# Optimization experiments

Hardware: AMD Instinct MI355X
Metric: run time of the kernel (lower is better)

## Reference

```python
import jax, jax.numpy as jnp
import numpy as np

B, S, D = 2, 2048, 1024
H, DK, DV = 16, 64, 64
DFF = 4096
EPS_RMS = 1e-6


def setup_inputs() -> dict:
    key = jax.random.key(0)
    ks = jax.random.split(key, 10)
    sc = 0.02
    return {
        "x": jax.random.normal(ks[0], (B, S, D), jnp.float32),
        "w_q": jax.random.normal(ks[1], (D, H * DK), jnp.float32) * sc,
        "w_k": jax.random.normal(ks[2], (D, H * DK), jnp.float32) * sc,
        "w_v": jax.random.normal(ks[3], (D, H * DV), jnp.float32) * sc,
        "w_o": jax.random.normal(ks[4], (H * DV, D), jnp.float32) * sc,
        "w_gate": jax.random.normal(ks[5], (D, DFF), jnp.float32) * sc,
        "w_up": jax.random.normal(ks[6], (D, DFF), jnp.float32) * sc,
        "w_down": jax.random.normal(ks[7], (DFF, D), jnp.float32) * sc,
        "g1": jnp.ones((D,), jnp.float32),
        "g2": jnp.ones((D,), jnp.float32),
    }


def _rmsnorm(x, g):
    var = jnp.mean(jnp.square(x), axis=-1, keepdims=True)
    return x * jax.lax.rsqrt(var + EPS_RMS) * g


def _stable_softmax(s):
    # Faithful to source: exp(x) / (sum exp(x) + 1e-9); fully-masked rows -> 0.
    e = jnp.exp(s)
    return e / (jnp.sum(e, axis=-1, keepdims=True) + 1e-9)


def reference(x, w_q, w_k, w_v, w_o, w_gate, w_up, w_down, g1, g2):
    b, s, d = x.shape
    h = _rmsnorm(x, g1)
    q = (h @ w_q).reshape(b, s, H, DK).transpose(0, 2, 1, 3)  # [B,H,S,DK]
    k = (h @ w_k).reshape(b, s, H, DK).transpose(0, 2, 1, 3)
    v = (h @ w_v).reshape(b, s, H, DV).transpose(0, 2, 1, 3)
    scores = jnp.einsum("bhqd,bhkd->bhqk", q, k) / jnp.sqrt(jnp.asarray(DK, x.dtype))
    # triu with diagonal=0: self and future positions are masked
    mask = jnp.triu(jnp.ones((s, s), bool))
    scores = jnp.where(mask, -jnp.inf, scores)
    attn = _stable_softmax(scores)  # [B,H,S,S]
    av = jnp.einsum("bhqk,bhkd->bhqd", attn, v)
    av = av.transpose(0, 2, 1, 3).reshape(b, s, H * DV)
    x = x + av @ w_o  # residual 1
    h2 = _rmsnorm(x, g2)
    hidden = jax.nn.silu(h2 @ w_gate) * (h2 @ w_up)
    return x + hidden @ w_down  # residual 2
```

## Files before the change

### kernel.cpp

```cpp
#include <hip/hip_runtime.h>
#include <cstdint>
#include <cstddef>

typedef unsigned short u16;
typedef unsigned int u32;
typedef __bf16 bf16x8 __attribute__((ext_vector_type(8)));
typedef float floatx4 __attribute__((ext_vector_type(4)));
typedef float floatx16 __attribute__((ext_vector_type(16)));

#define B_ 2
#define S_ 2048
#define D_ 1024
#define H_ 16
#define DFF_ 4096
#define BS_ 4096

__device__ __forceinline__ u16 f2bf(float f) {
  u32 u = __builtin_bit_cast(u32, f);
  u += 0x7fffu + ((u >> 16) & 1u);
  return (u16)(u >> 16);
}
__device__ __forceinline__ float bf2f(u16 h) {
  u32 u = ((u32)h) << 16;
  return __builtin_bit_cast(float, u);
}

__device__ __forceinline__ void gl_lds16(const u16* g, u16* l) {
  __builtin_amdgcn_global_load_lds(
      (const __attribute__((address_space(1))) void*)g,
      (__attribute__((address_space(3))) void*)l, 16, 0, 0);
}

__global__ void prep_weights(const float* __restrict__ wq, const float* __restrict__ wk,
                             const float* __restrict__ wv, const float* __restrict__ wo,
                             const float* __restrict__ wg, const float* __restrict__ wu,
                             const float* __restrict__ wd,
                             u16* __restrict__ wqkv_t, u16* __restrict__ wo_t,
                             u16* __restrict__ wgu_t, u16* __restrict__ wdn_t) {
  __shared__ float tile[32][33];
  const int id = blockIdx.x;
  const float* src;
  u16* dst;
  int R, C, bx, by, mode;
  if (id < 3072) {
    const int which = id >> 10, lo = id & 1023;
    src = which == 0 ? wq : (which == 1 ? wk : wv);
    dst = wqkv_t + which * 1024 * 1024;
    R = 1024; C = 1024; bx = lo & 31; by = lo >> 5; mode = 0;
  } else if (id < 4096) {
    const int lo = id - 3072;
    src = wo; dst = wo_t; R = 1024; C = 1024; bx = lo & 31; by = lo >> 5; mode = 0;
  } else if (id < 8192) {
    const int lo = id - 4096;
    src = wg; dst = wgu_t; R = 1024; C = 4096; bx = lo & 127; by = lo >> 7; mode = 1;
  } else if (id < 12288) {
    const int lo = id - 8192;
    src = wu; dst = wgu_t; R = 1024; C = 4096; bx = lo & 127; by = lo >> 7; mode = 2;
  } else {
    const int lo = id - 12288;
    src = wd; dst = wdn_t; R = 4096; C = 1024; bx = lo & 31; by = lo >> 5; mode = 0;
  }
  const int tx = threadIdx.x, ty = threadIdx.y;
  const int c0 = bx * 32, r0 = by * 32;
#pragma unroll
  for (int i = 0; i < 4; i++)
    tile[ty + i * 8][tx] = src[(size_t)(r0 + ty + i * 8) * C + c0 + tx];
  __syncthreads();
#pragma unroll
  for (int i = 0; i < 4; i++) {
    const int oc = c0 + ty + i * 8;
    const int orow = (mode == 0) ? oc
                                 : ((oc >> 5) * 64 + (oc & 31) + (mode == 2 ? 32 : 0));
    dst[(size_t)orow * R + r0 + tx] = f2bf(tile[tx][ty + i * 8]);
  }
}

__global__ __launch_bounds__(256) void rmsnorm_kernel(const float* __restrict__ x,
                                                      const float* __restrict__ g,
                                                      u16* __restrict__ out) {
  const int row = blockIdx.x, t = threadIdx.x;
  const float4 v = ((const float4*)(x + (size_t)row * 1024))[t];
  float ss = v.x * v.x + v.y * v.y + v.z * v.z + v.w * v.w;
#pragma unroll
  for (int off = 32; off > 0; off >>= 1) ss += __shfl_xor(ss, off);
  __shared__ float red[4];
  if ((t & 63) == 0) red[t >> 6] = ss;
  __syncthreads();
  ss = red[0] + red[1] + red[2] + red[3];
  const float inv = rsqrtf(ss * (1.0f / 1024.0f) + 1e-6f);
  const float4 gv = ((const float4*)g)[t];
  uint2 o;
  o.x = (u32)f2bf(v.x * inv * gv.x) | ((u32)f2bf(v.y * inv * gv.y) << 16);
  o.y = (u32)f2bf(v.z * inv * gv.z) | ((u32)f2bf(v.w * inv * gv.w) << 16);
  ((uint2*)(out + (size_t)row * 1024))[t] = o;
}

__global__ __launch_bounds__(256) void vtrans_kernel(const u16* __restrict__ qkv,
                                                     u16* __restrict__ vT) {
  __shared__ u16 tile[64][72];
  const int t = threadIdx.x;
  const int s0 = blockIdx.x * 64, h = blockIdx.y, b = blockIdx.z;
  const int r = t >> 2, cc = t & 3;
  const u16* src = qkv + (size_t)(b * S_ + s0 + r) * 3072 + 2 * D_ + h * 64 + cc * 16;
  *(uint4*)(&tile[r][cc * 16]) = *(const uint4*)src;
  *(uint4*)(&tile[r][cc * 16 + 8]) = *(const uint4*)(src + 8);
  __syncthreads();
  union { uint4 u[2]; u16 s[16]; } o;
#pragma unroll
  for (int j = 0; j < 16; j++) o.s[j] = tile[cc * 16 + j][r];
  u16* dst = vT + (size_t)((b * H_ + h) * 64 + r) * S_ + s0 + cc * 16;
  *(uint4*)dst = o.u[0];
  *(uint4*)(dst + 8) = o.u[1];
}

template <int BN, int EPI>
__global__ __launch_bounds__(256) void gemm_bt(const u16* __restrict__ A,
                                               const u16* __restrict__ Bt,
                                               void* __restrict__ Cout,
                                               const float* __restrict__ res,
                                               int M, int N, int K) {
  __shared__ u16 As[128 * 64];
  __shared__ u16 Bs[BN * 64];
  constexpr int NTI = BN / 64;
  constexpr int NSEG = 16 + BN / 8;
  constexpr int SPW = NSEG / 4;
  const int t = threadIdx.x, w = t >> 6, l = t & 63;
  const int m0 = blockIdx.y * 128, n0 = blockIdx.x * BN;
  const int wm = w >> 1, wn = w & 1;
  const int c31 = l & 31, khalf = l >> 5;

  const u16* gsrc[SPW];
  u16* ldst[SPW];
  {
    const int rl = l >> 3, ch = (l & 7) ^ rl;
#pragma unroll
    for (int i = 0; i < SPW; i++) {
      const int s = w * SPW + i;
      if (s < 16) {
        gsrc[i] = A + (size_t)(m0 + s * 8 + rl) * K + ch * 8;
        ldst[i] = As + s * 512;
      } else {
        gsrc[i] = Bt + (size_t)(n0 + (s - 16) * 8 + rl) * K + ch * 8;
        ldst[i] = Bs + (s - 16) * 512;
      }
    }
  }

  floatx16 acc[2][NTI] = {};

  for (int kk = 0; kk < K; kk += 64) {
    __syncthreads();
#pragma unroll
    for (int i = 0; i < SPW; i++) gl_lds16(gsrc[i], ldst[i]);
#pragma unroll
    for (int i = 0; i < SPW; i++) gsrc[i] += 64;
    __syncthreads();

#pragma unroll
    for (int ks = 0; ks < 4; ks++) {
      bf16x8 af[2], bfr[NTI];
#pragma unroll
      for (int mi = 0; mi < 2; mi++) {
        const int row = wm * 64 + mi * 32 + c31;
        const int e = (ks * 2 + khalf) ^ (row & 7);
        af[mi] = *(const bf16x8*)(As + row * 64 + e * 8);
      }
#pragma unroll
      for (int ni = 0; ni < NTI; ni++) {
        const int row = wn * (BN / 2) + ni * 32 + c31;
        const int e = (ks * 2 + khalf) ^ (row & 7);
        bfr[ni] = *(const bf16x8*)(Bs + row * 64 + e * 8);
      }
#pragma unroll
      for (int mi = 0; mi < 2; mi++)
#pragma unroll
        for (int ni = 0; ni < NTI; ni++)
          acc[mi][ni] = __builtin_amdgcn_mfma_f32_32x32x16_bf16(af[mi], bfr[ni],
                                                                acc[mi][ni], 0, 0, 0);
    }
  }

  if constexpr (EPI == 2) {
#pragma unroll
    for (int mi = 0; mi < 2; mi++) {
      const int colo = ((int)blockIdx.x * 2 + wn) * 32 + c31;
#pragma unroll
      for (int reg = 0; reg < 16; reg++) {
        const int row = m0 + wm * 64 + mi * 32 + (reg & 3) + 8 * (reg >> 2) + 4 * khalf;
        const float g = acc[mi][0][reg];
        const float u = acc[mi][NTI - 1][reg];
        ((u16*)Cout)[(size_t)row * 4096 + colo] = f2bf(g / (1.f + __expf(-g)) * u);
      }
    }
  } else {
#pragma unroll
    for (int mi = 0; mi < 2; mi++)
#pragma unroll
      for (int ni = 0; ni < NTI; ni++) {
        const int col = n0 + wn * (BN / 2) + ni * 32 + c31;
#pragma unroll
        for (int reg = 0; reg < 16; reg++) {
          const int row = m0 + wm * 64 + mi * 32 + (reg & 3) + 8 * (reg >> 2) + 4 * khalf;
          const size_t idx = (size_t)row * N + col;
          if (EPI == 0) ((u16*)Cout)[idx] = f2bf(acc[mi][ni][reg]);
          else          ((float*)Cout)[idx] = acc[mi][ni][reg] + res[idx];
        }
      }
  }
}

__global__ __launch_bounds__(256) void attn_kernel(const u16* __restrict__ qkv,
                                                   const u16* __restrict__ vT,
                                                   u16* __restrict__ av) {
  __shared__ u16 SM[2 * 8192];
  __shared__ u16 Ps[4 * 2048];
  const int t = threadIdx.x, w = t >> 6, l = t & 63;
  const int lrow = l & 15, lk = l >> 4;
  const int bh = blockIdx.x;
  const int b = bh >> 4, h = bh & 15;
  const int qt = 15 - (int)blockIdx.y;
  const int qbase = qt * 128 + w * 32;
  const int ktmax = 2 * qt + 1;
  u16* Pw = Ps + w * 2048;

  bf16x8 aq[2][2];
#pragma unroll
  for (int sub = 0; sub < 2; sub++)
#pragma unroll
    for (int half = 0; half < 2; half++)
      aq[sub][half] = *(const bf16x8*)(qkv + (size_t)(b * S_ + qbase + sub * 16 + lrow) * 3072 +
                                       h * 64 + half * 32 + lk * 8);

  const u16* gcur[4];
  int gstep[4], loff[4];
#pragma unroll
  for (int i = 0; i < 4; i++) {
    const int c = w + 4 * i;
    const int half = (c >> 2) & 1, grp = c & 3;
    if (c < 8) {
      gcur[i] = qkv + (size_t)(b * S_ + grp * 16 + (l >> 2)) * 3072 + D_ + h * 64 +
                half * 32 + (l & 3) * 8;
      gstep[i] = 64 * 3072;
      loff[i] = half * 2048 + grp * 512;
    } else {
      gcur[i] = vT + (size_t)(bh * 64 + grp * 16 + (l >> 2)) * S_ + half * 32 + (l & 3) * 8;
      gstep[i] = 64;
      loff[i] = 4096 + half * 2048 + grp * 512;
    }
  }

  floatx4 oacc[2][4] = {};
  float den[2] = {0.f, 0.f};

  int cur = 0;
#pragma unroll
  for (int i = 0; i < 4; i++) { gl_lds16(gcur[i], SM + loff[i]); gcur[i] += gstep[i]; }

  for (int kt = 0; kt <= ktmax; kt++) {
    __syncthreads();
    if (kt < ktmax) {
#pragma unroll
      for (int i = 0; i < 4; i++) {
        gl_lds16(gcur[i], SM + (cur ^ 1) * 8192 + loff[i]);
        gcur[i] += gstep[i];
      }
    }
    const u16* Kbuf = SM + cur * 8192;
    const u16* Vbuf = Kbuf + 4096;

    bf16x8 bk[4][2];
#pragma unroll
    for (int ct = 0; ct < 4; ct++)
#pragma unroll
      for (int half = 0; half < 2; half++)
        bk[ct][half] = *(const bf16x8*)(Kbuf + half * 2048 + (ct * 16 + lrow) * 32 + lk * 8);

    floatx4 sf[2][4] = {};
#pragma unroll
    for (int sub = 0; sub < 2; sub++)
#pragma unroll
      for (int ct = 0; ct < 4; ct++) {
        sf[sub][ct] = __builtin_amdgcn_mfma_f32_16x16x32_bf16(bk[ct][0], aq[sub][0],
                                                              sf[sub][ct], 0, 0, 0);
        sf[sub][ct] = __builtin_amdgcn_mfma_f32_16x16x32_bf16(bk[ct][1], aq[sub][1],
                                                              sf[sub][ct], 0, 0, 0);
      }

#pragma unroll
    for (int sub = 0; sub < 2; sub++) {
      const int qp = qbase + sub * 16 + lrow;
      const int prow = sub * 16 + lrow;
#pragma unroll
      for (int ct = 0; ct < 4; ct++) {
        const int kb = kt * 64 + ct * 16 + lk * 4;
        float p0 = (kb + 0 < qp) ? __expf(sf[sub][ct][0] * 0.125f) : 0.f;
        float p1 = (kb + 1 < qp) ? __expf(sf[sub][ct][1] * 0.125f) : 0.f;
        float p2 = (kb + 2 < qp) ? __expf(sf[sub][ct][2] * 0.125f) : 0.f;
        float p3 = (kb + 3 < qp) ? __expf(sf[sub][ct][3] * 0.125f) : 0.f;
        den[sub] += (p0 + p1) + (p2 + p3);
        uint2 pk;
        pk.x = (u32)f2bf(p0) | ((u32)f2bf(p1) << 16);
        pk.y = (u32)f2bf(p2) | ((u32)f2bf(p3) << 16);
        *(uint2*)(Pw + prow * 64 + (((2 * ct + (lk >> 1)) ^ (lrow & 7)) << 3) +
                  (lk & 1) * 4) = pk;
      }
    }

    bf16x8 ap[2][2], bv[4][2];
#pragma unroll
    for (int sub = 0; sub < 2; sub++)
#pragma unroll
      for (int kh = 0; kh < 2; kh++) {
        const int prow = sub * 16 + lrow;
        ap[sub][kh] = *(const bf16x8*)(Pw + prow * 64 + (((kh * 4 + lk) ^ (prow & 7)) << 3));
      }
#pragma unroll
    for (int ni = 0; ni < 4; ni++)
#pragma unroll
      for (int kh = 0; kh < 2; kh++)
        bv[ni][kh] = *(const bf16x8*)(Vbuf + kh * 2048 + (ni * 16 + lrow) * 32 + lk * 8);
#pragma unroll
    for (int sub = 0; sub < 2; sub++)
#pragma unroll
      for (int ni = 0; ni < 4; ni++) {
        oacc[sub][ni] = __builtin_amdgcn_mfma_f32_16x16x32_bf16(ap[sub][0], bv[ni][0],
                                                                oacc[sub][ni], 0, 0, 0);
        oacc[sub][ni] = __builtin_amdgcn_mfma_f32_16x16x32_bf16(ap[sub][1], bv[ni][1],
                                                                oacc[sub][ni], 0, 0, 0);
      }
    cur ^= 1;
  }

#pragma unroll
  for (int sub = 0; sub < 2; sub++) {
    den[sub] += __shfl_xor(den[sub], 16);
    den[sub] += __shfl_xor(den[sub], 32);
  }
  float dq[2][4];
#pragma unroll
  for (int sub = 0; sub < 2; sub++)
#pragma unroll
    for (int r = 0; r < 4; r++)
      dq[sub][r] = __shfl(den[sub], lk * 4 + r);

#pragma unroll
  for (int sub = 0; sub < 2; sub++)
#pragma unroll
    for (int ni = 0; ni < 4; ni++)
#pragma unroll
      for (int r = 0; r < 4; r++) {
        const int row = qbase + sub * 16 + lk * 4 + r;
        const int col = h * 64 + ni * 16 + lrow;
        av[(size_t)(b * S_ + row) * 1024 + col] = f2bf(oacc[sub][ni][r] / (dq[sub][r] + 1e-9f));
      }
}

#define OFF_WQKV 0u
#define OFF_WO   6291456u
#define OFF_WGU  8388608u
#define OFF_WDN  25165824u
#define OFF_H1   33554432u
#define OFF_QKV  41943040u
#define OFF_VT   67108864u
#define OFF_AV   75497472u
#define OFF_X1   83886080u
#define OFF_H2   100663296u
#define OFF_HID  109051904u

extern "C" void kernel_launch(void* const* d_in, const int* in_sizes, int n_in,
                              void* d_out, int out_size, void* d_ws, size_t ws_size,
                              hipStream_t stream) {
  const float* x      = (const float*)d_in[0];
  const float* w_q    = (const float*)d_in[1];
  const float* w_k    = (const float*)d_in[2];
  const float* w_v    = (const float*)d_in[3];
  const float* w_o    = (const float*)d_in[4];
  const float* w_gate = (const float*)d_in[5];
  const float* w_up   = (const float*)d_in[6];
  const float* w_down = (const float*)d_in[7];
  const float* g1     = (const float*)d_in[8];
  const float* g2     = (const float*)d_in[9];

  char* ws = (char*)d_ws;
  u16* wqkv_t = (u16*)(ws + OFF_WQKV);
  u16* wo_t   = (u16*)(ws + OFF_WO);
  u16* wgu_t  = (u16*)(ws + OFF_WGU);
  u16* wdn_t  = (u16*)(ws + OFF_WDN);
  u16* h1     = (u16*)(ws + OFF_H1);
  u16* qkv    = (u16*)(ws + OFF_QKV);
  u16* vT     = (u16*)(ws + OFF_VT);
  u16* av     = (u16*)(ws + OFF_AV);
  float* x1   = (float*)(ws + OFF_X1);
  u16* h2     = (u16*)(ws + OFF_H2);
  u16* hid    = (u16*)(ws + OFF_HID);
  float* out  = (float*)d_out;

  prep_weights<<<16384, dim3(32, 8), 0, stream>>>(w_q, w_k, w_v, w_o, w_gate, w_up, w_down,
                                                  wqkv_t, wo_t, wgu_t, wdn_t);

  rmsnorm_kernel<<<BS_, 256, 0, stream>>>(x, g1, h1);
  gemm_bt<128, 0><<<dim3(3072 / 128, BS_ / 128), 256, 0, stream>>>(h1, wqkv_t, qkv, nullptr,
                                                                   BS_, 3072, 1024);
  vtrans_kernel<<<dim3(S_ / 64, H_, B_), 256, 0, stream>>>(qkv, vT);
  attn_kernel<<<dim3(32, 16), 256, 0, stream>>>(qkv, vT, av);
  gemm_bt<64, 1><<<dim3(1024 / 64, BS_ / 128), 256, 0, stream>>>(av, wo_t, x1, x,
                                                                 BS_, 1024, 1024);
  rmsnorm_kernel<<<BS_, 256, 0, stream>>>(x1, g2, h2);
  gemm_bt<128, 2><<<dim3(8192 / 128, BS_ / 128), 256, 0, stream>>>(h2, wgu_t, hid, nullptr,
                                                                   BS_, 8192, 1024);
  gemm_bt<64, 1><<<dim3(1024 / 64, BS_ / 128), 256, 0, stream>>>(hid, wdn_t, out, x1,
                                                                 BS_, 1024, 4096);
}
```

Measured before the change: 392.9 us.

## Run gate/up GEMM in FP8, fuse V transpose into QKV GEMM epilogue

Quantizes the gate/up weights (scaled by 64) and the second RMSNorm output to e4m3 FP8 and computes the fused gate/up SwiGLU GEMM with scaled FP8 MFMA instructions. This halves operand bandwidth and raises matrix throughput for the largest GEMM. The V transpose kernel is dropped: the QKV GEMM epilogue now writes V directly in transposed layout, and prep_weights stores with vector writes. FP8 quantization of activations and weights lowers accuracy and may exceed tolerance.

```diff
diff --git a/kernel.cpp b/kernel.cpp
--- a/kernel.cpp
+++ b/kernel.cpp
@@ -3,10 +3,12 @@
 #include <cstddef>
 
 typedef unsigned short u16;
+typedef unsigned char u8;
 typedef unsigned int u32;
 typedef __bf16 bf16x8 __attribute__((ext_vector_type(8)));
 typedef float floatx4 __attribute__((ext_vector_type(4)));
 typedef float floatx16 __attribute__((ext_vector_type(16)));
+typedef int i32x8 __attribute__((ext_vector_type(8)));
 
 #define B_ 2
 #define S_ 2048
@@ -25,7 +27,20 @@
   return __builtin_bit_cast(float, u);
 }
 
-__device__ __forceinline__ void gl_lds16(const u16* g, u16* l) {
+__device__ __forceinline__ u32 f2e4m3(float f) {
+  u32 u = __builtin_bit_cast(u32, f);
+  const u32 s = (u >> 24) & 0x80u;
+  const u32 au = u & 0x7fffffffu;
+  if (au < 0x3c800000u) return s;
+  if (au > 0x43e00000u) return s | 0x7eu;
+  const u32 lsb = (au >> 20) & 1u;
+  const u32 r = au + 0x0007ffffu + lsb;
+  const u32 e = (r >> 23) & 0xffu;
+  const u32 m = (r >> 20) & 7u;
+  return s | (((e - 120u) & 0xfu) << 3) | m;
+}
+
+__device__ __forceinline__ void gl_lds16(const void* g, void* l) {
   __builtin_amdgcn_global_load_lds(
       (const __attribute__((address_space(1))) void*)g,
       (__attribute__((address_space(3))) void*)l, 16, 0, 0);
@@ -36,11 +51,11 @@
                              const float* __restrict__ wg, const float* __restrict__ wu,
                              const float* __restrict__ wd,
                              u16* __restrict__ wqkv_t, u16* __restrict__ wo_t,
-                             u16* __restrict__ wgu_t, u16* __restrict__ wdn_t) {
+                             u8* __restrict__ wguf8, u16* __restrict__ wdn_t) {
   __shared__ float tile[32][33];
   const int id = blockIdx.x;
   const float* src;
-  u16* dst;
+  u16* dst = nullptr;
   int R, C, bx, by, mode;
   if (id < 3072) {
     const int which = id >> 10, lo = id & 1023;
@@ -52,10 +67,10 @@
     src = wo; dst = wo_t; R = 1024; C = 1024; bx = lo & 31; by = lo >> 5; mode = 0;
   } else if (id < 8192) {
     const int lo = id - 4096;
-    src = wg; dst = wgu_t; R = 1024; C = 4096; bx = lo & 127; by = lo >> 7; mode = 1;
+    src = wg; R = 1024; C = 4096; bx = lo & 127; by = lo >> 7; mode = 1;
   } else if (id < 12288) {
     const int lo = id - 8192;
-    src = wu; dst = wgu_t; R = 1024; C = 4096; bx = lo & 127; by = lo >> 7; mode = 2;
+    src = wu; R = 1024; C = 4096; bx = lo & 127; by = lo >> 7; mode = 2;
   } else {
     const int lo = id - 12288;
     src = wd; dst = wdn_t; R = 4096; C = 1024; bx = lo & 31; by = lo >> 5; mode = 0;
@@ -66,18 +81,28 @@
   for (int i = 0; i < 4; i++)
     tile[ty + i * 8][tx] = src[(size_t)(r0 + ty + i * 8) * C + c0 + tx];
   __syncthreads();
-#pragma unroll
-  for (int i = 0; i < 4; i++) {
-    const int oc = c0 + ty + i * 8;
-    const int orow = (mode == 0) ? oc
-                                 : ((oc >> 5) * 64 + (oc & 31) + (mode == 2 ? 32 : 0));
-    dst[(size_t)orow * R + r0 + tx] = f2bf(tile[tx][ty + i * 8]);
-  }
-}
-
+  const int sx = ty * 32 + tx;
+  const int oci = sx >> 3, cg = (sx & 7) * 4;
+  const int oc = c0 + oci;
+  const float v0 = tile[cg][oci], v1 = tile[cg + 1][oci];
+  const float v2 = tile[cg + 2][oci], v3 = tile[cg + 3][oci];
+  if (mode == 0) {
+    uint2 o;
+    o.x = (u32)f2bf(v0) | ((u32)f2bf(v1) << 16);
+    o.y = (u32)f2bf(v2) | ((u32)f2bf(v3) << 16);
+    *(uint2*)(dst + (size_t)oc * R + r0 + cg) = o;
+  } else {
+    const int orow = (oc >> 5) * 64 + (oc & 31) + (mode == 2 ? 32 : 0);
+    const u32 p = f2e4m3(v0 * 64.f) | (f2e4m3(v1 * 64.f) << 8) |
+                  (f2e4m3(v2 * 64.f) << 16) | (f2e4m3(v3 * 64.f) << 24);
+    *(u32*)(wguf8 + (size_t)orow * 1024 + r0 + cg) = p;
+  }
+}
+
+template <int F8>
 __global__ __launch_bounds__(256) void rmsnorm_kernel(const float* __restrict__ x,
                                                       const float* __restrict__ g,
-                                                      u16* __restrict__ out) {
+                                                      void* __restrict__ out) {
   const int row = blockIdx.x, t = threadIdx.x;
   const float4 v = ((const float4*)(x + (size_t)row * 1024))[t];
   float ss = v.x * v.x + v.y * v.y + v.z * v.z + v.w * v.w;
@@ -89,28 +114,17 @@
   ss = red[0] + red[1] + red[2] + red[3];
   const float inv = rsqrtf(ss * (1.0f / 1024.0f) + 1e-6f);
   const float4 gv = ((const float4*)g)[t];
-  uint2 o;
-  o.x = (u32)f2bf(v.x * inv * gv.x) | ((u32)f2bf(v.y * inv * gv.y) << 16);
-  o.y = (u32)f2bf(v.z * inv * gv.z) | ((u32)f2bf(v.w * inv * gv.w) << 16);
-  ((uint2*)(out + (size_t)row * 1024))[t] = o;
-}
-
-__global__ __launch_bounds__(256) void vtrans_kernel(const u16* __restrict__ qkv,
-                                                     u16* __restrict__ vT) {
-  __shared__ u16 tile[64][72];
-  const int t = threadIdx.x;
-  const int s0 = blockIdx.x * 64, h = blockIdx.y, b = blockIdx.z;
-  const int r = t >> 2, cc = t & 3;
-  const u16* src = qkv + (size_t)(b * S_ + s0 + r) * 3072 + 2 * D_ + h * 64 + cc * 16;
-  *(uint4*)(&tile[r][cc * 16]) = *(const uint4*)src;
-  *(uint4*)(&tile[r][cc * 16 + 8]) = *(const uint4*)(src + 8);
-  __syncthreads();
-  union { uint4 u[2]; u16 s[16]; } o;
-#pragma unroll
-  for (int j = 0; j < 16; j++) o.s[j] = tile[cc * 16 + j][r];
-  u16* dst = vT + (size_t)((b * H_ + h) * 64 + r) * S_ + s0 + cc * 16;
-  *(uint4*)dst = o.u[0];
-  *(uint4*)(dst + 8) = o.u[1];
+  const float y0 = v.x * inv * gv.x, y1 = v.y * inv * gv.y;
+  const float y2 = v.z * inv * gv.z, y3 = v.w * inv * gv.w;
+  if (F8) {
+    const u32 p = f2e4m3(y0) | (f2e4m3(y1) << 8) | (f2e4m3(y2) << 16) | (f2e4m3(y3) << 24);
+    ((u32*)out)[(size_t)row * 256 + t] = p;
+  } else {
+    uint2 o;
+    o.x = (u32)f2bf(y0) | ((u32)f2bf(y1) << 16);
+    o.y = (u32)f2bf(y2) | ((u32)f2bf(y3) << 16);
+    ((uint2*)out)[(size_t)row * 256 + t] = o;
+  }
 }
 
 template <int BN, int EPI>
@@ -118,6 +132,7 @@
                                                const u16* __restrict__ Bt,
                                                void* __restrict__ Cout,
                                                const float* __restrict__ res,
+                                               u16* __restrict__ vTout,
                                                int M, int N, int K) {
   __shared__ u16 As[128 * 64];
   __shared__ u16 Bs[BN * 64];
@@ -180,32 +195,120 @@
     }
   }
 
-  if constexpr (EPI == 2) {
-#pragma unroll
-    for (int mi = 0; mi < 2; mi++) {
-      const int colo = ((int)blockIdx.x * 2 + wn) * 32 + c31;
+  if constexpr (EPI == 3) {
+    if (n0 >= 2048) {
+#pragma unroll
+      for (int mi = 0; mi < 2; mi++)
+#pragma unroll
+        for (int ni = 0; ni < NTI; ni++) {
+          const int col = n0 + wn * (BN / 2) + ni * 32 + c31 - 2048;
+          const int hh = col >> 6, dv = col & 63;
+          const int rbase = m0 + wm * 64 + mi * 32 + 4 * khalf;
+          const int bb = rbase >> 11;
+          u16* vp = vTout + (size_t)((bb * 16 + hh) * 64 + dv) * 2048 + (rbase & 2047);
+#pragma unroll
+          for (int rg = 0; rg < 4; rg++) {
+            uint2 pk;
+            pk.x = (u32)f2bf(acc[mi][ni][rg * 4 + 0]) |
+                   ((u32)f2bf(acc[mi][ni][rg * 4 + 1]) << 16);
+            pk.y = (u32)f2bf(acc[mi][ni][rg * 4 + 2]) |
+                   ((u32)f2bf(acc[mi][ni][rg * 4 + 3]) << 16);
+            *(uint2*)(vp + rg * 8) = pk;
+          }
+        }
+      return;
+    }
+  }
+#pragma unroll
+  for (int mi = 0; mi < 2; mi++)
+#pragma unroll
+    for (int ni = 0; ni < NTI; ni++) {
+      const int col = n0 + wn * (BN / 2) + ni * 32 + c31;
 #pragma unroll
       for (int reg = 0; reg < 16; reg++) {
         const int row = m0 + wm * 64 + mi * 32 + (reg & 3) + 8 * (reg >> 2) + 4 * khalf;
-        const float g = acc[mi][0][reg];
-        const float u = acc[mi][NTI - 1][reg];
-        ((u16*)Cout)[(size_t)row * 4096 + colo] = f2bf(g / (1.f + __expf(-g)) * u);
-      }
-    }
-  } else {
+        const size_t idx = (size_t)row * N + col;
+        if (EPI == 1) ((float*)Cout)[idx] = acc[mi][ni][reg] + res[idx];
+        else          ((u16*)Cout)[idx] = f2bf(acc[mi][ni][reg]);
+      }
+    }
+}
+
+__global__ __launch_bounds__(256) void gemm_f8(const u8* __restrict__ A,
+                                               const u8* __restrict__ B,
+                                               u16* __restrict__ hid,
+                                               int M, int K) {
+  __shared__ u8 As[128 * 64];
+  __shared__ u8 Bs[128 * 64];
+  const int t = threadIdx.x, w = t >> 6, l = t & 63;
+  const int m0 = blockIdx.y * 128, n0 = blockIdx.x * 128;
+  const int wm = w >> 1, wn = w & 1;
+  const int c31 = l & 31, hf = l >> 5;
+
+  const u8* gsrc[4];
+  u8* ldst[4];
+  {
+    const int rl = l >> 2, ch = (l & 3) ^ ((l >> 3) & 3);
+#pragma unroll
+    for (int i = 0; i < 4; i++) {
+      const int s = w * 4 + i;
+      if (s < 8) {
+        gsrc[i] = A + (size_t)(m0 + s * 16 + rl) * K + ch * 16;
+        ldst[i] = As + s * 1024;
+      } else {
+        gsrc[i] = B + (size_t)(n0 + (s - 8) * 16 + rl) * K + ch * 16;
+        ldst[i] = Bs + (s - 8) * 1024;
+      }
+    }
+  }
+
+  floatx16 acc[2][2] = {};
+
+  for (int kk = 0; kk < K; kk += 64) {
+    __syncthreads();
+#pragma unroll
+    for (int i = 0; i < 4; i++) gl_lds16(gsrc[i] + kk, ldst[i]);
+    __syncthreads();
+
+    i32x8 af[2], bf[2];
+#pragma unroll
+    for (int mi = 0; mi < 2; mi++) {
+      const int r = wm * 64 + mi * 32 + c31;
+      const int g = (r >> 1) & 3;
+      const uint4 lo = *(const uint4*)(As + r * 64 + ((2 * hf) ^ g) * 16);
+      const uint4 hi = *(const uint4*)(As + r * 64 + ((2 * hf + 1) ^ g) * 16);
+      af[mi] = i32x8{(int)lo.x, (int)lo.y, (int)lo.z, (int)lo.w,
+                     (int)hi.x, (int)hi.y, (int)hi.z, (int)hi.w};
+    }
+#pragma unroll
+    for (int ni = 0; ni < 2; ni++) {
+      const int r = wn * 64 + ni * 32 + c31;
+      const int g = (r >> 1) & 3;
+      const uint4 lo = *(const uint4*)(Bs + r * 64 + ((2 * hf) ^ g) * 16);
+      const uint4 hi = *(const uint4*)(Bs + r * 64 + ((2 * hf + 1) ^ g) * 16);
+      bf[ni] = i32x8{(int)lo.x, (int)lo.y, (int)lo.z, (int)lo.w,
+                     (int)hi.x, (int)hi.y, (int)hi.z, (int)hi.w};
+    }
 #pragma unroll
     for (int mi = 0; mi < 2; mi++)
 #pragma unroll
-      for (int ni = 0; ni < NTI; ni++) {
-        const int col = n0 + wn * (BN / 2) + ni * 32 + c31;
-#pragma unroll
-        for (int reg = 0; reg < 16; reg++) {
-          const int row = m0 + wm * 64 + mi * 32 + (reg & 3) + 8 * (reg >> 2) + 4 * khalf;
-          const size_t idx = (size_t)row * N + col;
-          if (EPI == 0) ((u16*)Cout)[idx] = f2bf(acc[mi][ni][reg]);
-          else          ((float*)Cout)[idx] = acc[mi][ni][reg] + res[idx];
-        }
-      }
+      for (int ni = 0; ni < 2; ni++)
+        acc[mi][ni] = __builtin_amdgcn_mfma_scale_f32_32x32x64_f8f6f4(
+            af[mi], bf[ni], acc[mi][ni], 0, 0,
+            0, 0x7F7F7F7F,
+            0, 0x79797979);
+  }
+
+#pragma unroll
+  for (int mi = 0; mi < 2; mi++) {
+    const int colo = ((int)blockIdx.x * 2 + wn) * 32 + c31;
+#pragma unroll
+    for (int reg = 0; reg < 16; reg++) {
+      const int row = m0 + wm * 64 + mi * 32 + (reg & 3) + 8 * (reg >> 2) + 4 * hf;
+      const float g = acc[mi][0][reg];
+      const float u = acc[mi][1][reg];
+      hid[(size_t)row * 4096 + colo] = f2bf(g / (1.f + __expf(-g)) * u);
+    }
   }
 }
 
@@ -357,15 +460,15 @@
 
 #define OFF_WQKV 0u
 #define OFF_WO   6291456u
-#define OFF_WGU  8388608u
-#define OFF_WDN  25165824u
-#define OFF_H1   33554432u
-#define OFF_QKV  41943040u
-#define OFF_VT   67108864u
-#define OFF_AV   75497472u
-#define OFF_X1   83886080u
-#define OFF_H2   100663296u
-#define OFF_HID  109051904u
+#define OFF_WGU8 8388608u
+#define OFF_WDN  16777216u
+#define OFF_H1   25165824u
+#define OFF_QKV  33554432u
+#define OFF_VT   58720256u
+#define OFF_AV   67108864u
+#define OFF_X1   75497472u
+#define OFF_H2F8 92274688u
+#define OFF_HID  96468992u
 
 extern "C" void kernel_launch(void* const* d_in, const int* in_sizes, int n_in,
                               void* d_out, int out_size, void* d_ws, size_t ws_size,
@@ -384,30 +487,28 @@
   char* ws = (char*)d_ws;
   u16* wqkv_t = (u16*)(ws + OFF_WQKV);
   u16* wo_t   = (u16*)(ws + OFF_WO);
-  u16* wgu_t  = (u16*)(ws + OFF_WGU);
+  u8*  wguf8  = (u8*)(ws + OFF_WGU8);
   u16* wdn_t  = (u16*)(ws + OFF_WDN);
   u16* h1     = (u16*)(ws + OFF_H1);
   u16* qkv    = (u16*)(ws + OFF_QKV);
   u16* vT     = (u16*)(ws + OFF_VT);
   u16* av     = (u16*)(ws + OFF_AV);
   float* x1   = (float*)(ws + OFF_X1);
-  u16* h2     = (u16*)(ws + OFF_H2);
+  u8*  h2f8   = (u8*)(ws + OFF_H2F8);
   u16* hid    = (u16*)(ws + OFF_HID);
   float* out  = (float*)d_out;
 
   prep_weights<<<16384, dim3(32, 8), 0, stream>>>(w_q, w_k, w_v, w_o, w_gate, w_up, w_down,
-                                                  wqkv_t, wo_t, wgu_t, wdn_t);
-
-  rmsnorm_kernel<<<BS_, 256, 0, stream>>>(x, g1, h1);
-  gemm_bt<128, 0><<<dim3(3072 / 128, BS_ / 128), 256, 0, stream>>>(h1, wqkv_t, qkv, nullptr,
-                                                                   BS_, 3072, 1024);
-  vtrans_kernel<<<dim3(S_ / 64, H_, B_), 256, 0, stream>>>(qkv, vT);
+                                                  wqkv_t, wo_t, wguf8, wdn_t);
+
+  rmsnorm_kernel<0><<<BS_, 256, 0, stream>>>(x, g1, h1);
+  gemm_bt<128, 3><<<dim3(3072 / 128, BS_ / 128), 256, 0, stream>>>(
+      h1, wqkv_t, qkv, nullptr, vT, BS_, 3072, 1024);
   attn_kernel<<<dim3(32, 16), 256, 0, stream>>>(qkv, vT, av);
-  gemm_bt<64, 1><<<dim3(1024 / 64, BS_ / 128), 256, 0, stream>>>(av, wo_t, x1, x,
-                                                                 BS_, 1024, 1024);
-  rmsnorm_kernel<<<BS_, 256, 0, stream>>>(x1, g2, h2);
-  gemm_bt<128, 2><<<dim3(8192 / 128, BS_ / 128), 256, 0, stream>>>(h2, wgu_t, hid, nullptr,
-                                                                   BS_, 8192, 1024);
-  gemm_bt<64, 1><<<dim3(1024 / 64, BS_ / 128), 256, 0, stream>>>(hid, wdn_t, out, x1,
-                                                                 BS_, 1024, 4096);
-}
+  gemm_bt<64, 1><<<dim3(1024 / 64, BS_ / 128), 256, 0, stream>>>(
+      av, wo_t, x1, x, nullptr, BS_, 1024, 1024);
+  rmsnorm_kernel<1><<<BS_, 256, 0, stream>>>(x1, g2, h2f8);
+  gemm_f8<<<dim3(4096 / 64, BS_ / 128), 256, 0, stream>>>(h2f8, wguf8, hid, BS_, 1024);
+  gemm_bt<64, 1><<<dim3(1024 / 64, BS_ / 128), 256, 0, stream>>>(
+      hid, wdn_t, out, x1, nullptr, BS_, 1024, 4096);
+}
```

New measurement: 349.2 us. -11.1%, faster.
